# Kernel tuning notes

Hardware: AMD Instinct MI355X
Metric: run time of the kernel (lower is better)

Reference implementation:

```python
import jax, jax.numpy as jnp
import numpy as np

THR = 1.0  # snntorch Leaky default threshold

# Heaviside spike with ATan surrogate gradient (snntorch surrogate.atan, alpha=2)
@jax.custom_vjp
def atan_spike(x):
    return (x > 0).astype(x.dtype)

def _spike_fwd(x):
    return atan_spike(x), x

def _spike_bwd(x, g):
    # d/dx of surrogate: (alpha/2) / (1 + (pi/2*alpha*x)^2) with alpha=2 -> 1/(1+(pi*x)^2)
    return (g / (1.0 + (jnp.pi * x) ** 2),)

atan_spike.defvjp(_spike_fwd, _spike_bwd)


def setup_inputs() -> dict:
    key = jax.random.key(0)
    ks = jax.random.split(key, 5)
    B, T = 256, 100
    D, H, O = 34 * 34 * 2, 1000, 10
    data = jax.random.normal(ks[0], (B, T, 2, 34, 34), jnp.float32)
    lim1 = 1.0 / np.sqrt(D)
    lim2 = 1.0 / np.sqrt(H)
    w1 = jax.random.uniform(ks[1], (H, D), jnp.float32, -lim1, lim1)
    b1 = jax.random.uniform(ks[2], (H,), jnp.float32, -lim1, lim1)
    w2 = jax.random.uniform(ks[3], (O, H), jnp.float32, -lim2, lim2)
    b2 = jax.random.uniform(ks[4], (O,), jnp.float32, -lim2, lim2)
    beta = jnp.float32(0.9)
    return {"data": data, "w1": w1, "b1": b1, "w2": w2, "b2": b2, "beta": beta}


def reference(data, w1, b1, w2, b2, beta):
    B, T = data.shape[0], data.shape[1]
    H, O = w1.shape[0], w2.shape[0]
    x = data.reshape(B, T, -1).transpose(1, 0, 2)  # [T, B, D] (Flatten per step)
    # Input currents to layer 1 are state-independent: one batched GEMM.
    cur1_all = jnp.einsum('tbd,hd->tbh', x, w1) + b1  # [T, B, H]

    mem1 = jnp.zeros((B, H), data.dtype)
    spk1 = jnp.zeros((B, H), data.dtype)
    mem2 = jnp.zeros((B, O), data.dtype)
    spk2 = jnp.zeros((B, O), data.dtype)

    def step(carry, cur1):
        mem1, spk1, mem2, spk2 = carry
        # snntorch Leaky, reset_mechanism='subtract':
        # mem = beta*mem + input - reset*threshold ; spk = fire(mem)
        mem1 = beta * mem1 + cur1 - spk1 * THR
        spk1 = atan_spike(mem1 - THR)
        cur2 = spk1 @ w2.T + b2
        mem2 = beta * mem2 + cur2 - spk2 * THR
        spk2 = atan_spike(mem2 - THR)
        return (mem1, spk1, mem2, spk2), (spk2, mem2)

    _, (spk_rec, mem_rec) = jax.lax.scan(step, (mem1, spk1, mem2, spk2), cur1_all)
    return spk_rec, mem_rec  # each [T, B, 10]
```

## Files before the change

kernel.cpp:

```cpp
#include <hip/hip_runtime.h>
#include <hip/hip_bf16.h>
#include <stdint.h>

#define T_STEPS 100
#define B_SZ    256
#define D_IN    2312
#define H_SZ    1000
#define O_SZ    10
#define M_ROWS  (B_SZ * T_STEPS)
#define K_PAD   2336
#define KT      73
#define W_ROWS  1024

#define A_SCALE   16.0f
#define W_SCALE   64.0f
#define INV_SCALE (1.0f / 1024.0f)

typedef __attribute__((ext_vector_type(4))) float     floatx4;
typedef __attribute__((ext_vector_type(8))) _Float16  halfx8;

#define ASYNC_COPY16(g, l)                                             \
  __builtin_amdgcn_global_load_lds(                                    \
      (const __attribute__((address_space(1))) void*)(g),              \
      (__attribute__((address_space(3))) void*)(l), 16, 0, 0)

__global__ __launch_bounds__(256)
void splitW_kernel(const float* __restrict__ W,
                   _Float16* __restrict__ wHi,
                   _Float16* __restrict__ wLo)
{
  const int r = blockIdx.x;
  const bool rvalid = (r < H_SZ);
  const float* w = W + (size_t)(rvalid ? r : 0) * D_IN;
  _Float16* ho = wHi + (size_t)r * K_PAD;
  _Float16* lo = wLo + (size_t)r * K_PAD;
  for (int c = threadIdx.x; c < K_PAD / 8; c += 256) {
    const int k0 = c * 8;
    const bool v = rvalid && (k0 + 8 <= D_IN);
    _Float16 h[8], l[8];
    #pragma unroll
    for (int e = 0; e < 8; ++e) {
      const float x = v ? w[k0 + e] * W_SCALE : 0.f;
      const _Float16 hb = (_Float16)x;
      h[e] = hb;
      l[e] = (_Float16)(x - (float)hb);
    }
    *reinterpret_cast<uint4*>(ho + k0) = *reinterpret_cast<const uint4*>(h);
    *reinterpret_cast<uint4*>(lo + k0) = *reinterpret_cast<const uint4*>(l);
  }
}

__global__ __launch_bounds__(512, 2)
void gemm1_fused(const float* __restrict__ A,
                 const _Float16* __restrict__ wHi,
                 const _Float16* __restrict__ wLo,
                 const float* __restrict__ b1,
                 float* __restrict__ C)
{
  __shared__ _Float16 sAh[2][256 * 32];
  __shared__ _Float16 sAl[2][256 * 32];
  __shared__ _Float16 sBh[2][256 * 32];
  __shared__ _Float16 sBl[2][256 * 32];

  const int tid  = threadIdx.x;

  const int id = blockIdx.x;
  const int l  = (id & 7) * 50 + (id >> 3);
  const int mt = l >> 2;
  const int nt = l & 3;
  const int m0 = mt * 256;
  const int n0 = nt * 256;

  const int wid  = tid >> 6;
  const int lane = tid & 63;
  const int wm   = (wid & 1) * 128;
  const int wn   = (wid >> 1) * 64;
  const int quad = lane >> 4;
  const int l16  = lane & 15;

  floatx4 acc[8][4];
  #pragma unroll
  for (int i = 0; i < 8; ++i)
    #pragma unroll
    for (int jj = 0; jj < 4; ++jj)
      acc[i][jj] = floatx4{0.f, 0.f, 0.f, 0.f};

  const int r0  = tid >> 2;
  const int r1  = r0 + 128;
  const int sl  = tid & 3;
  const int rho = (r0 >> 1) & 3;
  const int ko  = ((sl ^ rho) * 8);

  const float* gA0 = A + (size_t)(m0 + r0) * D_IN + ko;
  const float* gA1 = A + (size_t)(m0 + r1) * D_IN + ko;
  const _Float16* gBh0 = wHi + (size_t)(n0 + r0) * K_PAD + ko;
  const _Float16* gBh1 = wHi + (size_t)(n0 + r1) * K_PAD + ko;
  const _Float16* gBl0 = wLo + (size_t)(n0 + r0) * K_PAD + ko;
  const _Float16* gBl1 = wLo + (size_t)(n0 + r1) * K_PAD + ko;

  const int la0 = tid * 8;
  const int la1 = (tid + 512) * 8;

  const int fo = (quad ^ ((l16 >> 1) & 3)) * 8;

  float a0[8], a1[8];
  *reinterpret_cast<float4*>(a0)     = *reinterpret_cast<const float4*>(gA0);
  *reinterpret_cast<float4*>(a0 + 4) = *reinterpret_cast<const float4*>(gA0 + 4);
  *reinterpret_cast<float4*>(a1)     = *reinterpret_cast<const float4*>(gA1);
  *reinterpret_cast<float4*>(a1 + 4) = *reinterpret_cast<const float4*>(gA1 + 4);

  ASYNC_COPY16(gBh0, &sBh[0][la0]);
  ASYNC_COPY16(gBh1, &sBh[0][la1]);
  ASYNC_COPY16(gBl0, &sBl[0][la0]);
  ASYNC_COPY16(gBl1, &sBl[0][la1]);

  {
    _Float16 h0[8], l0[8], h1[8], l1[8];
    #pragma unroll
    for (int e = 0; e < 8; ++e) {
      const float v0 = a0[e] * A_SCALE;
      const _Float16 hb0 = (_Float16)v0;
      h0[e] = hb0; l0[e] = (_Float16)(v0 - (float)hb0);
      const float v1 = a1[e] * A_SCALE;
      const _Float16 hb1 = (_Float16)v1;
      h1[e] = hb1; l1[e] = (_Float16)(v1 - (float)hb1);
    }
    *reinterpret_cast<uint4*>(&sAh[0][la0]) = *reinterpret_cast<const uint4*>(h0);
    *reinterpret_cast<uint4*>(&sAl[0][la0]) = *reinterpret_cast<const uint4*>(l0);
    *reinterpret_cast<uint4*>(&sAh[0][la1]) = *reinterpret_cast<const uint4*>(h1);
    *reinterpret_cast<uint4*>(&sAl[0][la1]) = *reinterpret_cast<const uint4*>(l1);
  }

  *reinterpret_cast<float4*>(a0)     = *reinterpret_cast<const float4*>(gA0 + 32);
  *reinterpret_cast<float4*>(a0 + 4) = *reinterpret_cast<const float4*>(gA0 + 36);
  *reinterpret_cast<float4*>(a1)     = *reinterpret_cast<const float4*>(gA1 + 32);
  *reinterpret_cast<float4*>(a1 + 4) = *reinterpret_cast<const float4*>(gA1 + 36);
  bool curValid = true;

  for (int kt = 0; kt < KT; ++kt) {
    const int p = kt & 1;

    asm volatile("s_waitcnt vmcnt(4) lgkmcnt(0)" ::: "memory");
    __builtin_amdgcn_sched_barrier(0);
    __builtin_amdgcn_s_barrier();
    __builtin_amdgcn_sched_barrier(0);

    halfx8 bh[4], bl[4];
    #pragma unroll
    for (int jj = 0; jj < 4; ++jj) {
      const int row = (wn + jj * 16 + l16) * 32 + fo;
      bh[jj] = *reinterpret_cast<const halfx8*>(&sBh[p][row]);
      bl[jj] = *reinterpret_cast<const halfx8*>(&sBl[p][row]);
    }

    if (kt + 1 < KT) {
      _Float16 h0[8], l0[8], h1[8], l1[8];
      #pragma unroll
      for (int e = 0; e < 8; ++e) {
        const float v0 = curValid ? a0[e] * A_SCALE : 0.f;
        const _Float16 hb0 = (_Float16)v0;
        h0[e] = hb0; l0[e] = (_Float16)(v0 - (float)hb0);
        const float v1 = curValid ? a1[e] * A_SCALE : 0.f;
        const _Float16 hb1 = (_Float16)v1;
        h1[e] = hb1; l1[e] = (_Float16)(v1 - (float)hb1);
      }
      const int q = p ^ 1;
      *reinterpret_cast<uint4*>(&sAh[q][la0]) = *reinterpret_cast<const uint4*>(h0);
      *reinterpret_cast<uint4*>(&sAl[q][la0]) = *reinterpret_cast<const uint4*>(l0);
      *reinterpret_cast<uint4*>(&sAh[q][la1]) = *reinterpret_cast<const uint4*>(h1);
      *reinterpret_cast<uint4*>(&sAl[q][la1]) = *reinterpret_cast<const uint4*>(l1);

      const int kb = (kt + 1) * 32;
      ASYNC_COPY16(gBh0 + kb, &sBh[q][la0]);
      ASYNC_COPY16(gBh1 + kb, &sBh[q][la1]);
      ASYNC_COPY16(gBl0 + kb, &sBl[q][la0]);
      ASYNC_COPY16(gBl1 + kb, &sBl[q][la1]);

      const int kb2 = (kt + 2) * 32;
      const bool v = (kb2 + ko) < D_IN;
      const int off = v ? kb2 : 0;
      *reinterpret_cast<float4*>(a0)     = *reinterpret_cast<const float4*>(gA0 + off);
      *reinterpret_cast<float4*>(a0 + 4) = *reinterpret_cast<const float4*>(gA0 + off + 4);
      *reinterpret_cast<float4*>(a1)     = *reinterpret_cast<const float4*>(gA1 + off);
      *reinterpret_cast<float4*>(a1 + 4) = *reinterpret_cast<const float4*>(gA1 + off + 4);
      curValid = v;
    }

    __builtin_amdgcn_s_setprio(1);
    #pragma unroll
    for (int i = 0; i < 8; ++i) {
      const int row = (wm + i * 16 + l16) * 32 + fo;
      const halfx8 ah = *reinterpret_cast<const halfx8*>(&sAh[p][row]);
      const halfx8 al = *reinterpret_cast<const halfx8*>(&sAl[p][row]);
      #pragma unroll
      for (int jj = 0; jj < 4; ++jj) {
        acc[i][jj] = __builtin_amdgcn_mfma_f32_16x16x32_f16(ah, bh[jj], acc[i][jj], 0, 0, 0);
        acc[i][jj] = __builtin_amdgcn_mfma_f32_16x16x32_f16(al, bh[jj], acc[i][jj], 0, 0, 0);
        acc[i][jj] = __builtin_amdgcn_mfma_f32_16x16x32_f16(ah, bl[jj], acc[i][jj], 0, 0, 0);
      }
    }
    __builtin_amdgcn_s_setprio(0);
  }

  #pragma unroll
  for (int jj = 0; jj < 4; ++jj) {
    const int col = n0 + wn + jj * 16 + l16;
    if (col < H_SZ) {
      const float bias = b1[col];
      #pragma unroll
      for (int i = 0; i < 8; ++i) {
        const int row = m0 + wm + i * 16 + quad * 4;
        #pragma unroll
        for (int r = 0; r < 4; ++r)
          C[(size_t)(row + r) * H_SZ + col] = acc[i][jj][r] * INV_SCALE + bias;
      }
    }
  }
}

__global__ __launch_bounds__(256)
void scan1_kernel(const float* __restrict__ cur1,
                  const float* __restrict__ beta_p,
                  __hip_bfloat16* __restrict__ spk1)
{
  const int h = blockIdx.x * 256 + threadIdx.x;
  const int b = blockIdx.y;
  if (h >= H_SZ) return;
  const float beta = beta_p[0];
  const float* c    = cur1 + (size_t)b * T_STEPS * H_SZ + h;
  __hip_bfloat16* s = spk1 + (size_t)b * T_STEPS * H_SZ + h;
  float mem = 0.f, spk = 0.f;
  #pragma unroll 4
  for (int t = 0; t < T_STEPS; ++t) {
    mem = beta * mem + c[(size_t)t * H_SZ] - spk;
    spk = (mem > 1.0f) ? 1.0f : 0.0f;
    s[(size_t)t * H_SZ] = __float2bfloat16(spk);
  }
}

__global__ __launch_bounds__(256)
void gemm2_kernel(const __hip_bfloat16* __restrict__ spk1,
                  const float* __restrict__ w2,
                  float* __restrict__ cur2)
{
  const int wid  = threadIdx.x >> 6;
  const int lane = threadIdx.x & 63;
  const int m    = blockIdx.x * 4 + wid;

  float acc[O_SZ];
  #pragma unroll
  for (int o = 0; o < O_SZ; ++o) acc[o] = 0.f;

  const __hip_bfloat16* row = spk1 + (size_t)m * H_SZ;
  #pragma unroll
  for (int it = 0; it < 16; ++it) {
    const int h = it * 64 + lane;
    if (h < H_SZ) {
      const float s = __bfloat162float(row[h]);
      if (s != 0.f) {
        #pragma unroll
        for (int o = 0; o < O_SZ; ++o)
          acc[o] += w2[o * H_SZ + h];
      }
    }
  }
  #pragma unroll
  for (int o = 0; o < O_SZ; ++o) {
    float v = acc[o];
    #pragma unroll
    for (int off = 32; off > 0; off >>= 1) v += __shfl_down(v, off);
    if (lane == 0) cur2[(size_t)m * O_SZ + o] = v;
  }
}

__global__ __launch_bounds__(256)
void scan2_kernel(const float* __restrict__ cur2,
                  const float* __restrict__ b2,
                  const float* __restrict__ beta_p,
                  float* __restrict__ out)
{
  const int idx = blockIdx.x * 256 + threadIdx.x;
  if (idx >= B_SZ * O_SZ) return;
  const int b = idx / O_SZ;
  const int o = idx % O_SZ;
  const float beta = beta_p[0];
  const float bias = b2[o];
  float* spk_rec = out;
  float* mem_rec = out + (size_t)T_STEPS * B_SZ * O_SZ;
  float mem = 0.f, spk = 0.f;
  for (int t = 0; t < T_STEPS; ++t) {
    const float cur = cur2[((size_t)b * T_STEPS + t) * O_SZ + o] + bias;
    mem = beta * mem + cur - spk;
    spk = (mem > 1.0f) ? 1.0f : 0.0f;
    const size_t oi = ((size_t)t * B_SZ + b) * O_SZ + o;
    spk_rec[oi] = spk;
    mem_rec[oi] = mem;
  }
}

extern "C" void kernel_launch(void* const* d_in, const int* in_sizes, int n_in,
                              void* d_out, int out_size, void* d_ws, size_t ws_size,
                              hipStream_t stream)
{
  const float* data = (const float*)d_in[0];
  const float* w1   = (const float*)d_in[1];
  const float* b1   = (const float*)d_in[2];
  const float* w2   = (const float*)d_in[3];
  const float* b2   = (const float*)d_in[4];
  const float* beta = (const float*)d_in[5];
  float* out = (float*)d_out;

  char* p = (char*)d_ws;
  auto take = [&](size_t n) { char* q = p; p += (n + 255) & ~(size_t)255; return q; };
  _Float16*       wHi  = (_Float16*)take((size_t)W_ROWS * K_PAD * 2);
  _Float16*       wLo  = (_Float16*)take((size_t)W_ROWS * K_PAD * 2);
  float*          cur1 = (float*)take((size_t)M_ROWS * H_SZ * 4);
  __hip_bfloat16* spk1 = (__hip_bfloat16*)take((size_t)M_ROWS * H_SZ * 2);
  float*          cur2 = (float*)take((size_t)M_ROWS * O_SZ * 4);

  splitW_kernel<<<dim3(W_ROWS), 256, 0, stream>>>(w1, wHi, wLo);
  gemm1_fused<<<dim3(400), 512, 0, stream>>>(data, wHi, wLo, b1, cur1);
  scan1_kernel<<<dim3(4, B_SZ), 256, 0, stream>>>(cur1, beta, spk1);
  gemm2_kernel<<<dim3(M_ROWS / 4), 256, 0, stream>>>(spk1, w2, cur2);
  scan2_kernel<<<dim3(10), 256, 0, stream>>>(cur2, b2, beta, out);
}
```

Measured before the change: 763.6 us.

## Interleave GEMM1 LDS staging mid-MFMA loop and bit-pack spike matrix

Inside the GEMM1 main loop, the A fp16 hi/lo split and store and the B async copies are placed halfway through the MFMA sequence, and the next A global load is moved after the MFMAs. The intent is to overlap staging work with matrix math. Separately, scan1 now writes spikes as 64-bit ballot masks instead of a bf16 matrix, and gemm2 reads those masks. This cuts intermediate memory traffic, but the rescheduling may lengthen load latency exposure.

```diff
diff --git a/kernel.cpp b/kernel.cpp
--- a/kernel.cpp
+++ b/kernel.cpp
@@ -153,42 +153,36 @@
       bl[jj] = *reinterpret_cast<const halfx8*>(&sBl[p][row]);
     }
 
-    if (kt + 1 < KT) {
-      _Float16 h0[8], l0[8], h1[8], l1[8];
-      #pragma unroll
-      for (int e = 0; e < 8; ++e) {
-        const float v0 = curValid ? a0[e] * A_SCALE : 0.f;
-        const _Float16 hb0 = (_Float16)v0;
-        h0[e] = hb0; l0[e] = (_Float16)(v0 - (float)hb0);
-        const float v1 = curValid ? a1[e] * A_SCALE : 0.f;
-        const _Float16 hb1 = (_Float16)v1;
-        h1[e] = hb1; l1[e] = (_Float16)(v1 - (float)hb1);
+    __builtin_amdgcn_s_setprio(1);
+    #pragma unroll
+    for (int i = 0; i < 8; ++i) {
+      if (i == 4) {
+        __builtin_amdgcn_s_setprio(0);
+        if (kt + 1 < KT) {
+          _Float16 h0[8], l0[8], h1[8], l1[8];
+          #pragma unroll
+          for (int e = 0; e < 8; ++e) {
+            const float v0 = curValid ? a0[e] * A_SCALE : 0.f;
+            const _Float16 hb0 = (_Float16)v0;
+            h0[e] = hb0; l0[e] = (_Float16)(v0 - (float)hb0);
+            const float v1 = curValid ? a1[e] * A_SCALE : 0.f;
+            const _Float16 hb1 = (_Float16)v1;
+            h1[e] = hb1; l1[e] = (_Float16)(v1 - (float)hb1);
+          }
+          const int q = p ^ 1;
+          *reinterpret_cast<uint4*>(&sAh[q][la0]) = *reinterpret_cast<const uint4*>(h0);
+          *reinterpret_cast<uint4*>(&sAl[q][la0]) = *reinterpret_cast<const uint4*>(l0);
+          *reinterpret_cast<uint4*>(&sAh[q][la1]) = *reinterpret_cast<const uint4*>(h1);
+          *reinterpret_cast<uint4*>(&sAl[q][la1]) = *reinterpret_cast<const uint4*>(l1);
+
+          const int kb = (kt + 1) * 32;
+          ASYNC_COPY16(gBh0 + kb, &sBh[q][la0]);
+          ASYNC_COPY16(gBh1 + kb, &sBh[q][la1]);
+          ASYNC_COPY16(gBl0 + kb, &sBl[q][la0]);
+          ASYNC_COPY16(gBl1 + kb, &sBl[q][la1]);
+        }
+        __builtin_amdgcn_s_setprio(1);
       }
-      const int q = p ^ 1;
-      *reinterpret_cast<uint4*>(&sAh[q][la0]) = *reinterpret_cast<const uint4*>(h0);
-      *reinterpret_cast<uint4*>(&sAl[q][la0]) = *reinterpret_cast<const uint4*>(l0);
-      *reinterpret_cast<uint4*>(&sAh[q][la1]) = *reinterpret_cast<const uint4*>(h1);
-      *reinterpret_cast<uint4*>(&sAl[q][la1]) = *reinterpret_cast<const uint4*>(l1);
-
-      const int kb = (kt + 1) * 32;
-      ASYNC_COPY16(gBh0 + kb, &sBh[q][la0]);
-      ASYNC_COPY16(gBh1 + kb, &sBh[q][la1]);
-      ASYNC_COPY16(gBl0 + kb, &sBl[q][la0]);
-      ASYNC_COPY16(gBl1 + kb, &sBl[q][la1]);
-
-      const int kb2 = (kt + 2) * 32;
-      const bool v = (kb2 + ko) < D_IN;
-      const int off = v ? kb2 : 0;
-      *reinterpret_cast<float4*>(a0)     = *reinterpret_cast<const float4*>(gA0 + off);
-      *reinterpret_cast<float4*>(a0 + 4) = *reinterpret_cast<const float4*>(gA0 + off + 4);
-      *reinterpret_cast<float4*>(a1)     = *reinterpret_cast<const float4*>(gA1 + off);
-      *reinterpret_cast<float4*>(a1 + 4) = *reinterpret_cast<const float4*>(gA1 + off + 4);
-      curValid = v;
-    }
-
-    __builtin_amdgcn_s_setprio(1);
-    #pragma unroll
-    for (int i = 0; i < 8; ++i) {
       const int row = (wm + i * 16 + l16) * 32 + fo;
       const halfx8 ah = *reinterpret_cast<const halfx8*>(&sAh[p][row]);
       const halfx8 al = *reinterpret_cast<const halfx8*>(&sAl[p][row]);
@@ -200,6 +194,17 @@
       }
     }
     __builtin_amdgcn_s_setprio(0);
+
+    if (kt + 1 < KT) {
+      const int kb2 = (kt + 2) * 32;
+      const bool v = (kb2 + ko) < D_IN;
+      const int off = v ? kb2 : 0;
+      *reinterpret_cast<float4*>(a0)     = *reinterpret_cast<const float4*>(gA0 + off);
+      *reinterpret_cast<float4*>(a0 + 4) = *reinterpret_cast<const float4*>(gA0 + off + 4);
+      *reinterpret_cast<float4*>(a1)     = *reinterpret_cast<const float4*>(gA1 + off);
+      *reinterpret_cast<float4*>(a1 + 4) = *reinterpret_cast<const float4*>(gA1 + off + 4);
+      curValid = v;
+    }
   }
 
   #pragma unroll
@@ -221,25 +226,28 @@
 __global__ __launch_bounds__(256)
 void scan1_kernel(const float* __restrict__ cur1,
                   const float* __restrict__ beta_p,
-                  __hip_bfloat16* __restrict__ spk1)
+                  unsigned long long* __restrict__ spkbits)
 {
   const int h = blockIdx.x * 256 + threadIdx.x;
   const int b = blockIdx.y;
   if (h >= H_SZ) return;
+  const int g    = h >> 6;
+  const int lane = threadIdx.x & 63;
   const float beta = beta_p[0];
-  const float* c    = cur1 + (size_t)b * T_STEPS * H_SZ + h;
-  __hip_bfloat16* s = spk1 + (size_t)b * T_STEPS * H_SZ + h;
+  const float* c = cur1 + (size_t)b * T_STEPS * H_SZ + h;
   float mem = 0.f, spk = 0.f;
   #pragma unroll 4
   for (int t = 0; t < T_STEPS; ++t) {
     mem = beta * mem + c[(size_t)t * H_SZ] - spk;
     spk = (mem > 1.0f) ? 1.0f : 0.0f;
-    s[(size_t)t * H_SZ] = __float2bfloat16(spk);
+    const unsigned long long mask = __ballot(spk != 0.f);
+    if (lane == 0)
+      spkbits[((size_t)b * T_STEPS + t) * 16 + g] = mask;
   }
 }
 
 __global__ __launch_bounds__(256)
-void gemm2_kernel(const __hip_bfloat16* __restrict__ spk1,
+void gemm2_kernel(const unsigned long long* __restrict__ spkbits,
                   const float* __restrict__ w2,
                   float* __restrict__ cur2)
 {
@@ -251,18 +259,16 @@
   #pragma unroll
   for (int o = 0; o < O_SZ; ++o) acc[o] = 0.f;
 
-  const __hip_bfloat16* row = spk1 + (size_t)m * H_SZ;
-  #pragma unroll
-  for (int it = 0; it < 16; ++it) {
-    const int h = it * 64 + lane;
-    if (h < H_SZ) {
-      const float s = __bfloat162float(row[h]);
-      if (s != 0.f) {
-        #pragma unroll
-        for (int o = 0; o < O_SZ; ++o)
-          acc[o] += w2[o * H_SZ + h];
-      }
-    }
+  const unsigned long long* bits = spkbits + (size_t)m * 16;
+  #pragma unroll
+  for (int g = 0; g < 16; ++g) {
+    const unsigned long long mask = bits[g];
+    const float s = (float)((mask >> lane) & 1ull);
+    const int h  = g * 64 + lane;
+    const int hc = (h < H_SZ) ? h : (H_SZ - 1);
+    #pragma unroll
+    for (int o = 0; o < O_SZ; ++o)
+      acc[o] = fmaf(s, w2[o * H_SZ + hc], acc[o]);
   }
   #pragma unroll
   for (int o = 0; o < O_SZ; ++o) {
@@ -312,15 +318,15 @@
 
   char* p = (char*)d_ws;
   auto take = [&](size_t n) { char* q = p; p += (n + 255) & ~(size_t)255; return q; };
-  _Float16*       wHi  = (_Float16*)take((size_t)W_ROWS * K_PAD * 2);
-  _Float16*       wLo  = (_Float16*)take((size_t)W_ROWS * K_PAD * 2);
-  float*          cur1 = (float*)take((size_t)M_ROWS * H_SZ * 4);
-  __hip_bfloat16* spk1 = (__hip_bfloat16*)take((size_t)M_ROWS * H_SZ * 2);
-  float*          cur2 = (float*)take((size_t)M_ROWS * O_SZ * 4);
+  _Float16*           wHi     = (_Float16*)take((size_t)W_ROWS * K_PAD * 2);
+  _Float16*           wLo     = (_Float16*)take((size_t)W_ROWS * K_PAD * 2);
+  float*              cur1    = (float*)take((size_t)M_ROWS * H_SZ * 4);
+  unsigned long long* spkbits = (unsigned long long*)take((size_t)M_ROWS * 16 * 8);
+  float*              cur2    = (float*)take((size_t)M_ROWS * O_SZ * 4);
 
   splitW_kernel<<<dim3(W_ROWS), 256, 0, stream>>>(w1, wHi, wLo);
   gemm1_fused<<<dim3(400), 512, 0, stream>>>(data, wHi, wLo, b1, cur1);
-  scan1_kernel<<<dim3(4, B_SZ), 256, 0, stream>>>(cur1, beta, spk1);
-  gemm2_kernel<<<dim3(M_ROWS / 4), 256, 0, stream>>>(spk1, w2, cur2);
+  scan1_kernel<<<dim3(4, B_SZ), 256, 0, stream>>>(cur1, beta, spkbits);
+  gemm2_kernel<<<dim3(M_ROWS / 4), 256, 0, stream>>>(spkbits, w2, cur2);
   scan2_kernel<<<dim3(10), 256, 0, stream>>>(cur2, b2, beta, out);
 }
```

Measured after the change: 731.7 us. -4.2%, faster.
